# Performance work log

Hardware: AMD Instinct MI355X
Metric: run time of the kernel (lower is better)

Reference implementation:

```python
import jax, jax.numpy as jnp
import numpy as np

EPS = 1e-8  # torch nn.CosineSimilarity default eps


def setup_inputs() -> dict:
    key = jax.random.key(0)
    k1, k2 = jax.random.split(key)
    text_encodings = jax.random.normal(k1, (65536, 256), dtype=jnp.float32)
    label_encodings = jax.random.normal(k2, (1024, 256), dtype=jnp.float32)
    return {"text_encodings": text_encodings, "label_encodings": label_encodings}


def reference(text_encodings, label_encodings):
    # cosine_sim(x, y) = x.y / max(||x||*||y||, eps), computed as one matmul
    dots = jnp.einsum('nd,ld->nl', text_encodings, label_encodings)  # [N, L]
    tn = jnp.linalg.norm(text_encodings, axis=-1)    # [N]
    ln = jnp.linalg.norm(label_encodings, axis=-1)   # [L]
    denom = jnp.maximum(tn[:, None] * ln[None, :], EPS)
    return dots / denom
```

## Files before the change

kernel.cpp:

```cpp
#include <hip/hip_runtime.h>
#include <hip/hip_bf16.h>

#define NT 65536
#define NL 1024
#define DD 256

#define BM 128
#define BN 128
#define BK 64

typedef __attribute__((ext_vector_type(4))) float f32x4;
typedef __attribute__((ext_vector_type(8))) short bf16x8;

__device__ inline short f2bf(float x) {
    union { __hip_bfloat16 b; short s; } u;
    u.b = __float2bfloat16(x);
    return u.s;
}

__global__ __launch_bounds__(256) void norms_k(const float* __restrict__ A,
                                               const float* __restrict__ Bm,
                                               float* __restrict__ rt,
                                               float* __restrict__ rl) {
    int gw   = (blockIdx.x * 256 + threadIdx.x) >> 6;
    int lane = threadIdx.x & 63;
    if (gw >= NT + NL) return;
    const float* src = (gw < NT) ? (A + (size_t)gw * DD)
                                 : (Bm + (size_t)(gw - NT) * DD);
    float4 v = reinterpret_cast<const float4*>(src)[lane];
    float s = v.x * v.x + v.y * v.y + v.z * v.z + v.w * v.w;
#pragma unroll
    for (int off = 32; off > 0; off >>= 1) s += __shfl_xor(s, off);
    if (lane == 0) {
        float n = sqrtf(s);
        float r = 1.0f / fmaxf(n, 1e-20f);
        if (gw < NT) rt[gw] = r; else rl[gw - NT] = r;
    }
}

__global__ __launch_bounds__(256, 2) void cosim_k(const float* __restrict__ A,
                                                  const float* __restrict__ Bm,
                                                  const float* __restrict__ rt,
                                                  const float* __restrict__ rl,
                                                  float* __restrict__ C) {
    __shared__ short As[BM * BK];
    __shared__ short Bs[BN * BK];

    const int tid  = threadIdx.x;
    const int lane = tid & 63;
    const int wid  = tid >> 6;
    const int wr   = wid >> 1;
    const int wc   = wid & 1;

    const int orig = blockIdx.x;
    const int id   = (orig & 7) * (4096 / 8) + (orig >> 3);
    const int bx   = id & 7;
    const int by   = id >> 3;

    const int m0 = by * BM;
    const int l0 = bx * BN;

    const int srow = tid >> 4;
    const int sc4  = tid & 15;

    f32x4 ra[8], rb[8];

    auto loadg = [&](int kt) {
        const float* pa = A  + (size_t)m0 * DD + kt * BK;
        const float* pb = Bm + (size_t)l0 * DD + kt * BK;
#pragma unroll
        for (int i = 0; i < 8; ++i) {
            int row = srow + i * 16;
            ra[i] = reinterpret_cast<const f32x4*>(pa + (size_t)row * DD)[sc4];
            rb[i] = reinterpret_cast<const f32x4*>(pb + (size_t)row * DD)[sc4];
        }
    };

    auto stash = [&]() {
#pragma unroll
        for (int i = 0; i < 8; ++i) {
            int row = srow + i * 16;
            short4 pa, pb;
            pa.x = f2bf(ra[i].x); pa.y = f2bf(ra[i].y);
            pa.z = f2bf(ra[i].z); pa.w = f2bf(ra[i].w);
            pb.x = f2bf(rb[i].x); pb.y = f2bf(rb[i].y);
            pb.z = f2bf(rb[i].z); pb.w = f2bf(rb[i].w);
            *reinterpret_cast<short4*>(&As[row * BK + sc4 * 4]) = pa;
            *reinterpret_cast<short4*>(&Bs[row * BK + sc4 * 4]) = pb;
        }
    };

    f32x4 acc[4][4] = {};

    loadg(0);
#pragma unroll
    for (int kt = 0; kt < DD / BK; ++kt) {
        __syncthreads();
        stash();
        __syncthreads();
        if (kt < DD / BK - 1) loadg(kt + 1);
#pragma unroll
        for (int ks = 0; ks < 2; ++ks) {
            bf16x8 af[4], bfr[4];
            const int kof = ks * 32 + (lane >> 4) * 8;
            const int ar  = wr * 64 + (lane & 15);
            const int bc  = wc * 64 + (lane & 15);
#pragma unroll
            for (int i = 0; i < 4; ++i)
                af[i] = *reinterpret_cast<const bf16x8*>(&As[(ar + i * 16) * BK + kof]);
#pragma unroll
            for (int j = 0; j < 4; ++j)
                bfr[j] = *reinterpret_cast<const bf16x8*>(&Bs[(bc + j * 16) * BK + kof]);
#pragma unroll
            for (int i = 0; i < 4; ++i)
#pragma unroll
                for (int j = 0; j < 4; ++j)
                    acc[i][j] = __builtin_amdgcn_mfma_f32_16x16x32_bf16(
                        af[i], bfr[j], acc[i][j], 0, 0, 0);
        }
    }

    const int crow0 = m0 + wr * 64;
    const int ccol0 = l0 + wc * 64;
    const int rq = lane >> 4;
    const int cc = lane & 15;
#pragma unroll
    for (int i = 0; i < 4; ++i) {
#pragma unroll
        for (int r = 0; r < 4; ++r) {
            int row = crow0 + i * 16 + rq * 4 + r;
            float rsc = rt[row];
            float* crow = C + (size_t)row * NL;
#pragma unroll
            for (int j = 0; j < 4; ++j) {
                int col = ccol0 + j * 16 + cc;
                crow[col] = acc[i][j][r] * rsc * rl[col];
            }
        }
    }
}

extern "C" void kernel_launch(void* const* d_in, const int* in_sizes, int n_in,
                              void* d_out, int out_size, void* d_ws, size_t ws_size,
                              hipStream_t stream) {
    const float* A  = (const float*)d_in[0];
    const float* Bm = (const float*)d_in[1];
    float* C  = (float*)d_out;
    float* rt = (float*)d_ws;
    float* rl = rt + NT;

    norms_k<<<(NT + NL) / 4, 256, 0, stream>>>(A, Bm, rt, rl);

    dim3 grid(NL / BN * NT / BM);
    cosim_k<<<grid, 256, 0, stream>>>(A, Bm, rt, rl, C);
}
```

Baseline: 349.0 us.

## Pre-convert inputs to bf16 and stream tiles via direct global-to-LDS loads

A prep kernel now converts both fp32 inputs to bf16 in workspace while computing the inverse norms. The GEMM kernel then loads bf16 tiles straight into LDS with global_load_lds and an XOR swizzle, removing per-tile fp32 loads, register staging and in-kernel conversion. This halves the bytes each tile re-reads and raises occupancy to 3 blocks per CU. In exchange it adds an extra write and read of a bf16 copy of A, and the main loop keeps no register prefetch overlap. The old path is kept as a fallback for when the workspace is too small.

```diff
diff --git a/kernel.cpp b/kernel.cpp
--- a/kernel.cpp
+++ b/kernel.cpp
@@ -16,6 +16,121 @@
     union { __hip_bfloat16 b; short s; } u;
     u.b = __float2bfloat16(x);
     return u.s;
+}
+
+__device__ inline void gload_lds16(const void* g, void* l) {
+    __builtin_amdgcn_global_load_lds((const __attribute__((address_space(1))) void*)g,
+                                     (__attribute__((address_space(3))) void*)l,
+                                     16, 0, 0);
+}
+
+__global__ __launch_bounds__(256) void prep_k(const float* __restrict__ A,
+                                              const float* __restrict__ Bm,
+                                              short* __restrict__ Abf,
+                                              short* __restrict__ Bbf,
+                                              float* __restrict__ rt,
+                                              float* __restrict__ rl) {
+    int gw   = (blockIdx.x * 256 + threadIdx.x) >> 6;
+    int lane = threadIdx.x & 63;
+    if (gw >= NT + NL) return;
+    const float* src = (gw < NT) ? (A + (size_t)gw * DD) : (Bm + (size_t)(gw - NT) * DD);
+    short*       dst = (gw < NT) ? (Abf + (size_t)gw * DD) : (Bbf + (size_t)(gw - NT) * DD);
+    float4 v = reinterpret_cast<const float4*>(src)[lane];
+    short4 o;
+    o.x = f2bf(v.x); o.y = f2bf(v.y); o.z = f2bf(v.z); o.w = f2bf(v.w);
+    reinterpret_cast<short4*>(dst)[lane] = o;
+    float s = v.x * v.x + v.y * v.y + v.z * v.z + v.w * v.w;
+#pragma unroll
+    for (int off = 32; off > 0; off >>= 1) s += __shfl_xor(s, off);
+    if (lane == 0) {
+        float r = 1.0f / fmaxf(sqrtf(s), 1e-20f);
+        if (gw < NT) rt[gw] = r; else rl[gw - NT] = r;
+    }
+}
+
+__global__ __launch_bounds__(256, 3) void cosim_bf_k(const short* __restrict__ Abf,
+                                                     const short* __restrict__ Bbf,
+                                                     const float* __restrict__ rt,
+                                                     const float* __restrict__ rl,
+                                                     float* __restrict__ C) {
+    __shared__ short As[BM * BK];
+    __shared__ short Bs[BN * BK];
+
+    const int tid  = threadIdx.x;
+    const int lane = tid & 63;
+    const int w    = tid >> 6;
+    const int wr   = w >> 1;
+    const int wc   = w & 1;
+
+    const int orig = blockIdx.x;
+    const int id   = (orig & 7) * (4096 / 8) + (orig >> 3);
+    const int bx   = id & 7;
+    const int by   = id >> 3;
+    const int m0   = by * BM;
+    const int l0   = bx * BN;
+
+    const int l8 = lane >> 3;
+    const int ch = lane & 7;
+    const int cg = ch ^ l8;
+
+    f32x4 acc[4][4] = {};
+
+#pragma unroll
+    for (int kt = 0; kt < DD / BK; ++kt) {
+        __syncthreads();
+#pragma unroll
+        for (int i = 0; i < 4; ++i) {
+            int r = w * 32 + i * 8 + l8;
+            gload_lds16(Abf + (size_t)(m0 + r) * DD + kt * BK + cg * 8,
+                        &As[(w * 32 + i * 8) * BK]);
+            gload_lds16(Bbf + (size_t)(l0 + r) * DD + kt * BK + cg * 8,
+                        &Bs[(w * 32 + i * 8) * BK]);
+        }
+        __syncthreads();
+#pragma unroll
+        for (int ks = 0; ks < 2; ++ks) {
+            bf16x8 af[4], bfr[4];
+            const int fr = lane & 15;
+            const int fq = lane >> 4;
+#pragma unroll
+            for (int i = 0; i < 4; ++i) {
+                int row = wr * 64 + i * 16 + fr;
+                int ck  = (ks * 4 + fq) ^ (row & 7);
+                af[i] = *reinterpret_cast<const bf16x8*>(&As[row * BK + ck * 8]);
+            }
+#pragma unroll
+            for (int j = 0; j < 4; ++j) {
+                int row = wc * 64 + j * 16 + fr;
+                int ck  = (ks * 4 + fq) ^ (row & 7);
+                bfr[j] = *reinterpret_cast<const bf16x8*>(&Bs[row * BK + ck * 8]);
+            }
+#pragma unroll
+            for (int i = 0; i < 4; ++i)
+#pragma unroll
+                for (int j = 0; j < 4; ++j)
+                    acc[i][j] = __builtin_amdgcn_mfma_f32_16x16x32_bf16(
+                        af[i], bfr[j], acc[i][j], 0, 0, 0);
+        }
+    }
+
+    const int crow0 = m0 + wr * 64;
+    const int ccol0 = l0 + wc * 64;
+    const int rq = lane >> 4;
+    const int cc = lane & 15;
+#pragma unroll
+    for (int i = 0; i < 4; ++i) {
+#pragma unroll
+        for (int r = 0; r < 4; ++r) {
+            int row = crow0 + i * 16 + rq * 4 + r;
+            float rsc = rt[row];
+            float* crow = C + (size_t)row * NL;
+#pragma unroll
+            for (int j = 0; j < 4; ++j) {
+                int col = ccol0 + j * 16 + cc;
+                crow[col] = acc[i][j][r] * rsc * rl[col];
+            }
+        }
+    }
 }
 
 __global__ __launch_bounds__(256) void norms_k(const float* __restrict__ A,
@@ -25,46 +140,38 @@
     int gw   = (blockIdx.x * 256 + threadIdx.x) >> 6;
     int lane = threadIdx.x & 63;
     if (gw >= NT + NL) return;
-    const float* src = (gw < NT) ? (A + (size_t)gw * DD)
-                                 : (Bm + (size_t)(gw - NT) * DD);
+    const float* src = (gw < NT) ? (A + (size_t)gw * DD) : (Bm + (size_t)(gw - NT) * DD);
     float4 v = reinterpret_cast<const float4*>(src)[lane];
     float s = v.x * v.x + v.y * v.y + v.z * v.z + v.w * v.w;
 #pragma unroll
     for (int off = 32; off > 0; off >>= 1) s += __shfl_xor(s, off);
     if (lane == 0) {
-        float n = sqrtf(s);
-        float r = 1.0f / fmaxf(n, 1e-20f);
+        float r = 1.0f / fmaxf(sqrtf(s), 1e-20f);
         if (gw < NT) rt[gw] = r; else rl[gw - NT] = r;
     }
 }
 
-__global__ __launch_bounds__(256, 2) void cosim_k(const float* __restrict__ A,
-                                                  const float* __restrict__ Bm,
-                                                  const float* __restrict__ rt,
-                                                  const float* __restrict__ rl,
-                                                  float* __restrict__ C) {
+__global__ __launch_bounds__(256, 2) void cosim_fused_k(const float* __restrict__ A,
+                                                        const float* __restrict__ Bm,
+                                                        const float* __restrict__ rt,
+                                                        const float* __restrict__ rl,
+                                                        float* __restrict__ C) {
     __shared__ short As[BM * BK];
     __shared__ short Bs[BN * BK];
-
     const int tid  = threadIdx.x;
     const int lane = tid & 63;
     const int wid  = tid >> 6;
     const int wr   = wid >> 1;
     const int wc   = wid & 1;
-
     const int orig = blockIdx.x;
     const int id   = (orig & 7) * (4096 / 8) + (orig >> 3);
     const int bx   = id & 7;
     const int by   = id >> 3;
-
     const int m0 = by * BM;
     const int l0 = bx * BN;
-
     const int srow = tid >> 4;
     const int sc4  = tid & 15;
-
     f32x4 ra[8], rb[8];
-
     auto loadg = [&](int kt) {
         const float* pa = A  + (size_t)m0 * DD + kt * BK;
         const float* pb = Bm + (size_t)l0 * DD + kt * BK;
@@ -75,7 +182,6 @@
             rb[i] = reinterpret_cast<const f32x4*>(pb + (size_t)row * DD)[sc4];
         }
     };
-
     auto stash = [&]() {
 #pragma unroll
         for (int i = 0; i < 8; ++i) {
@@ -89,9 +195,7 @@
             *reinterpret_cast<short4*>(&Bs[row * BK + sc4 * 4]) = pb;
         }
     };
-
     f32x4 acc[4][4] = {};
-
     loadg(0);
 #pragma unroll
     for (int kt = 0; kt < DD / BK; ++kt) {
@@ -119,7 +223,6 @@
                         af[i], bfr[j], acc[i][j], 0, 0, 0);
         }
     }
-
     const int crow0 = m0 + wr * 64;
     const int ccol0 = l0 + wc * 64;
     const int rq = lane >> 4;
@@ -145,12 +248,24 @@
                               hipStream_t stream) {
     const float* A  = (const float*)d_in[0];
     const float* Bm = (const float*)d_in[1];
-    float* C  = (float*)d_out;
-    float* rt = (float*)d_ws;
-    float* rl = rt + NT;
-
-    norms_k<<<(NT + NL) / 4, 256, 0, stream>>>(A, Bm, rt, rl);
-
-    dim3 grid(NL / BN * NT / BM);
-    cosim_k<<<grid, 256, 0, stream>>>(A, Bm, rt, rl, C);
-}
+    float* C = (float*)d_out;
+
+    const size_t abf_elems = (size_t)NT * DD;
+    const size_t bbf_elems = (size_t)NL * DD;
+    const size_t need = (abf_elems + bbf_elems) * sizeof(short)
+                      + (NT + NL) * sizeof(float);
+
+    if (ws_size >= need) {
+        short* Abf = (short*)d_ws;
+        short* Bbf = Abf + abf_elems;
+        float* rt  = (float*)(Bbf + bbf_elems);
+        float* rl  = rt + NT;
+        prep_k<<<(NT + NL) / 4, 256, 0, stream>>>(A, Bm, Abf, Bbf, rt, rl);
+        cosim_bf_k<<<(NL / BN) * (NT / BM), 256, 0, stream>>>(Abf, Bbf, rt, rl, C);
+    } else {
+        float* rt = (float*)d_ws;
+        float* rl = rt + NT;
+        norms_k<<<(NT + NL) / 4, 256, 0, stream>>>(A, Bm, rt, rl);
+        cosim_fused_k<<<(NL / BN) * (NT / BM), 256, 0, stream>>>(A, Bm, rt, rl, C);
+    }
+}
```

Result: faster. 340.1 us (-2.5%).

## Fuse norm computation into GEMM kernel, use 8 waves and swizzled LDS

Applied to the files above, without the earlier changes.

Drops the separate norms kernel. Each GEMM block now accumulates the squared norms of its A and B rows from the fp32 tiles it already loads, reduces them with shuffles and keeps the reciprocals in LDS for the epilogue. The block grows to 512 threads (8 waves, each computing 64x32), and LDS stores and reads use an XOR swizzle to avoid bank conflicts. The cost is that every block recomputes norms for rows other blocks also use, and the deeper pipeline is replaced by a simpler single-buffer loop with two barriers per k-step.

```diff
diff --git a/kernel.cpp b/kernel.cpp
--- a/kernel.cpp
+++ b/kernel.cpp
@@ -18,123 +18,129 @@
     return u.s;
 }
 
-__global__ __launch_bounds__(256) void norms_k(const float* __restrict__ A,
-                                               const float* __restrict__ Bm,
-                                               float* __restrict__ rt,
-                                               float* __restrict__ rl) {
-    int gw   = (blockIdx.x * 256 + threadIdx.x) >> 6;
-    int lane = threadIdx.x & 63;
-    if (gw >= NT + NL) return;
-    const float* src = (gw < NT) ? (A + (size_t)gw * DD)
-                                 : (Bm + (size_t)(gw - NT) * DD);
-    float4 v = reinterpret_cast<const float4*>(src)[lane];
-    float s = v.x * v.x + v.y * v.y + v.z * v.z + v.w * v.w;
-#pragma unroll
-    for (int off = 32; off > 0; off >>= 1) s += __shfl_xor(s, off);
-    if (lane == 0) {
-        float n = sqrtf(s);
-        float r = 1.0f / fmaxf(n, 1e-20f);
-        if (gw < NT) rt[gw] = r; else rl[gw - NT] = r;
-    }
-}
-
-__global__ __launch_bounds__(256, 2) void cosim_k(const float* __restrict__ A,
+__global__ __launch_bounds__(512, 4) void cosim_k(const float* __restrict__ A,
                                                   const float* __restrict__ Bm,
-                                                  const float* __restrict__ rt,
-                                                  const float* __restrict__ rl,
                                                   float* __restrict__ C) {
     __shared__ short As[BM * BK];
     __shared__ short Bs[BN * BK];
+    __shared__ float rnA[BM];
+    __shared__ float rnB[BN];
 
     const int tid  = threadIdx.x;
     const int lane = tid & 63;
-    const int wid  = tid >> 6;
-    const int wr   = wid >> 1;
-    const int wc   = wid & 1;
+    const int w    = tid >> 6;
+    const int wr   = w >> 2;
+    const int wc   = w & 3;
 
     const int orig = blockIdx.x;
     const int id   = (orig & 7) * (4096 / 8) + (orig >> 3);
     const int bx   = id & 7;
     const int by   = id >> 3;
+    const int m0   = by * BM;
+    const int l0   = bx * BN;
 
-    const int m0 = by * BM;
-    const int l0 = bx * BN;
+    const int sr  = tid >> 3;
+    const int sch = tid & 7;
+    const int scs = sch ^ (sr & 7);
 
-    const int srow = tid >> 4;
-    const int sc4  = tid & 15;
+    const float* Ap0 = A  + (size_t)(m0 + sr)      * DD + sch * 8;
+    const float* Ap1 = A  + (size_t)(m0 + sr + 64) * DD + sch * 8;
+    const float* Bp0 = Bm + (size_t)(l0 + sr)      * DD + sch * 8;
+    const float* Bp1 = Bm + (size_t)(l0 + sr + 64) * DD + sch * 8;
 
-    f32x4 ra[8], rb[8];
+    f32x4 a00, a01, a10, a11, b00, b01, b10, b11;
+    float sa0 = 0.f, sa1 = 0.f, sb0 = 0.f, sb1 = 0.f;
 
-    auto loadg = [&](int kt) {
-        const float* pa = A  + (size_t)m0 * DD + kt * BK;
-        const float* pb = Bm + (size_t)l0 * DD + kt * BK;
-#pragma unroll
-        for (int i = 0; i < 8; ++i) {
-            int row = srow + i * 16;
-            ra[i] = reinterpret_cast<const f32x4*>(pa + (size_t)row * DD)[sc4];
-            rb[i] = reinterpret_cast<const f32x4*>(pb + (size_t)row * DD)[sc4];
-        }
+    auto ldregs = [&](int kt) {
+        const f32x4* pa0 = reinterpret_cast<const f32x4*>(Ap0 + kt * BK);
+        const f32x4* pa1 = reinterpret_cast<const f32x4*>(Ap1 + kt * BK);
+        const f32x4* pb0 = reinterpret_cast<const f32x4*>(Bp0 + kt * BK);
+        const f32x4* pb1 = reinterpret_cast<const f32x4*>(Bp1 + kt * BK);
+        a00 = pa0[0]; a01 = pa0[1];
+        a10 = pa1[0]; a11 = pa1[1];
+        b00 = pb0[0]; b01 = pb0[1];
+        b10 = pb1[0]; b11 = pb1[1];
+    };
+    auto sq8 = [](f32x4 lo, f32x4 hi) {
+        return lo[0]*lo[0] + lo[1]*lo[1] + lo[2]*lo[2] + lo[3]*lo[3]
+             + hi[0]*hi[0] + hi[1]*hi[1] + hi[2]*hi[2] + hi[3]*hi[3];
+    };
+    auto cvt8 = [](f32x4 lo, f32x4 hi) {
+        bf16x8 r;
+        r[0] = f2bf(lo[0]); r[1] = f2bf(lo[1]); r[2] = f2bf(lo[2]); r[3] = f2bf(lo[3]);
+        r[4] = f2bf(hi[0]); r[5] = f2bf(hi[1]); r[6] = f2bf(hi[2]); r[7] = f2bf(hi[3]);
+        return r;
     };
 
-    auto stash = [&]() {
-#pragma unroll
-        for (int i = 0; i < 8; ++i) {
-            int row = srow + i * 16;
-            short4 pa, pb;
-            pa.x = f2bf(ra[i].x); pa.y = f2bf(ra[i].y);
-            pa.z = f2bf(ra[i].z); pa.w = f2bf(ra[i].w);
-            pb.x = f2bf(rb[i].x); pb.y = f2bf(rb[i].y);
-            pb.z = f2bf(rb[i].z); pb.w = f2bf(rb[i].w);
-            *reinterpret_cast<short4*>(&As[row * BK + sc4 * 4]) = pa;
-            *reinterpret_cast<short4*>(&Bs[row * BK + sc4 * 4]) = pb;
-        }
-    };
+    const int fr = lane & 15;
+    const int fq = lane >> 4;
+    f32x4 acc[4][2] = {};
 
-    f32x4 acc[4][4] = {};
-
-    loadg(0);
+    ldregs(0);
 #pragma unroll
     for (int kt = 0; kt < DD / BK; ++kt) {
+        sa0 += sq8(a00, a01);  sa1 += sq8(a10, a11);
+        sb0 += sq8(b00, b01);  sb1 += sq8(b10, b11);
+        *reinterpret_cast<bf16x8*>(&As[sr        * BK + scs * 8]) = cvt8(a00, a01);
+        *reinterpret_cast<bf16x8*>(&As[(sr + 64) * BK + scs * 8]) = cvt8(a10, a11);
+        *reinterpret_cast<bf16x8*>(&Bs[sr        * BK + scs * 8]) = cvt8(b00, b01);
+        *reinterpret_cast<bf16x8*>(&Bs[(sr + 64) * BK + scs * 8]) = cvt8(b10, b11);
+        if (kt < DD / BK - 1) ldregs(kt + 1);
         __syncthreads();
-        stash();
-        __syncthreads();
-        if (kt < DD / BK - 1) loadg(kt + 1);
+
 #pragma unroll
         for (int ks = 0; ks < 2; ++ks) {
-            bf16x8 af[4], bfr[4];
-            const int kof = ks * 32 + (lane >> 4) * 8;
-            const int ar  = wr * 64 + (lane & 15);
-            const int bc  = wc * 64 + (lane & 15);
+            bf16x8 af[4], bfr[2];
 #pragma unroll
-            for (int i = 0; i < 4; ++i)
-                af[i] = *reinterpret_cast<const bf16x8*>(&As[(ar + i * 16) * BK + kof]);
+            for (int i = 0; i < 4; ++i) {
+                int row = wr * 64 + i * 16 + fr;
+                int ck  = (ks * 4 + fq) ^ (row & 7);
+                af[i] = *reinterpret_cast<const bf16x8*>(&As[row * BK + ck * 8]);
+            }
 #pragma unroll
-            for (int j = 0; j < 4; ++j)
-                bfr[j] = *reinterpret_cast<const bf16x8*>(&Bs[(bc + j * 16) * BK + kof]);
+            for (int j = 0; j < 2; ++j) {
+                int row = wc * 32 + j * 16 + fr;
+                int ck  = (ks * 4 + fq) ^ (row & 7);
+                bfr[j] = *reinterpret_cast<const bf16x8*>(&Bs[row * BK + ck * 8]);
+            }
 #pragma unroll
             for (int i = 0; i < 4; ++i)
 #pragma unroll
-                for (int j = 0; j < 4; ++j)
+                for (int j = 0; j < 2; ++j)
                     acc[i][j] = __builtin_amdgcn_mfma_f32_16x16x32_bf16(
                         af[i], bfr[j], acc[i][j], 0, 0, 0);
         }
+        __syncthreads();
     }
 
-    const int crow0 = m0 + wr * 64;
-    const int ccol0 = l0 + wc * 64;
+#pragma unroll
+    for (int off = 1; off < 8; off <<= 1) {
+        sa0 += __shfl_xor(sa0, off);
+        sa1 += __shfl_xor(sa1, off);
+        sb0 += __shfl_xor(sb0, off);
+        sb1 += __shfl_xor(sb1, off);
+    }
+    if (sch == 0) {
+        rnA[sr]      = 1.0f / fmaxf(sqrtf(sa0), 1e-20f);
+        rnA[sr + 64] = 1.0f / fmaxf(sqrtf(sa1), 1e-20f);
+        rnB[sr]      = 1.0f / fmaxf(sqrtf(sb0), 1e-20f);
+        rnB[sr + 64] = 1.0f / fmaxf(sqrtf(sb1), 1e-20f);
+    }
+    __syncthreads();
+
     const int rq = lane >> 4;
     const int cc = lane & 15;
 #pragma unroll
     for (int i = 0; i < 4; ++i) {
 #pragma unroll
-        for (int r = 0; r < 4; ++r) {
-            int row = crow0 + i * 16 + rq * 4 + r;
-            float rsc = rt[row];
-            float* crow = C + (size_t)row * NL;
+        for (int rr = 0; rr < 4; ++rr) {
+            int lr = wr * 64 + i * 16 + rq * 4 + rr;
+            float rsc = rnA[lr];
+            float* crow = C + (size_t)(m0 + lr) * NL + l0;
 #pragma unroll
-            for (int j = 0; j < 4; ++j) {
-                int col = ccol0 + j * 16 + cc;
-                crow[col] = acc[i][j][r] * rsc * rl[col];
+            for (int j = 0; j < 2; ++j) {
+                int lc = wc * 32 + j * 16 + cc;
+                crow[lc] = acc[i][j][rr] * rsc * rnB[lc];
             }
         }
     }
@@ -145,12 +151,8 @@
                               hipStream_t stream) {
     const float* A  = (const float*)d_in[0];
     const float* Bm = (const float*)d_in[1];
-    float* C  = (float*)d_out;
-    float* rt = (float*)d_ws;
-    float* rl = rt + NT;
+    float* C = (float*)d_out;
+    (void)d_ws; (void)ws_size;
 
-    norms_k<<<(NT + NL) / 4, 256, 0, stream>>>(A, Bm, rt, rl);
-
-    dim3 grid(NL / BN * NT / BM);
-    cosim_k<<<grid, 256, 0, stream>>>(A, Bm, rt, rl, C);
+    cosim_k<<<(NL / BN) * (NT / BM), 512, 0, stream>>>(A, Bm, C);
 }
```

New measurement: 379.6 us. 8.8% more time.
